# Performance work log

Hardware: AMD Instinct MI355X
Metric: run time of the kernel (lower is better)

The kernel has to match this reference:

```python
import jax, jax.numpy as jnp
import numpy as np

EMBED_DIM = 1024
NUM_HEADS = 16
HEAD_DIM = EMBED_DIM // NUM_HEADS


def setup_inputs() -> dict:
    key = jax.random.key(0)
    ks = jax.random.split(key, 9)
    B, S, E, H, D = 4, 1024, EMBED_DIM, NUM_HEADS, HEAD_DIM
    s = 1.0 / np.sqrt(E)
    return {
        "input_ids": jax.random.normal(ks[0], (B, S, E), dtype=jnp.float32),
        # stacked per-head projection weights, [H, E, D] (x @ W convention)
        "W_q": jax.random.normal(ks[1], (H, E, D), dtype=jnp.float32) * s,
        "b_q": jax.random.normal(ks[2], (H, D), dtype=jnp.float32) * 0.02,
        "W_k": jax.random.normal(ks[3], (H, E, D), dtype=jnp.float32) * s,
        "b_k": jax.random.normal(ks[4], (H, D), dtype=jnp.float32) * 0.02,
        # v_net exists in the module but is UNUSED (bug: v = q_net(x)); kept for faithfulness
        "W_v": jax.random.normal(ks[5], (H, E, D), dtype=jnp.float32) * s,
        "b_v": jax.random.normal(ks[6], (H, D), dtype=jnp.float32) * 0.02,
        "W_o": jax.random.normal(ks[7], (E, E), dtype=jnp.float32) * s,
        "b_o": jax.random.normal(ks[8], (E,), dtype=jnp.float32) * 0.02,
    }


def reference(input_ids, W_q, b_q, W_k, b_k, W_v, b_v, W_o, b_o):
    B, S, E = input_ids.shape
    # per-head projections, batched across heads: [B, H, S, D]
    q = jnp.einsum("bse,hed->bhsd", input_ids, W_q) + b_q[None, :, None, :]
    k = jnp.einsum("bse,hed->bhsd", input_ids, W_k) + b_k[None, :, None, :]
    v = q  # faithful to original bug: v = self.q_net(input_ids)
    # faithful to original: scale by sqrt(seq_len) (q.shape[1] of [B,S,D]), not sqrt(head_dim)
    scores = jnp.einsum("bhqd,bhkd->bhqk", q, k) / jnp.sqrt(jnp.asarray(S, input_ids.dtype))
    # faithful to original: softmax over dim=1 of [B, Sq, Sk] -> the query axis (axis=2 here)
    attn = jax.nn.softmax(scores, axis=2)
    out = jnp.einsum("bhqk,bhkd->bhqd", attn, v)  # [B, H, S, D]
    out = out.transpose(0, 2, 1, 3).reshape(B, S, E)  # concat heads
    return out @ W_o + b_o
```

## Files before the change

### kernel.cpp

```cpp
#include <hip/hip_runtime.h>
#include <cstddef>

typedef __attribute__((ext_vector_type(8))) short bf16x8;
typedef __attribute__((ext_vector_type(4))) float f32x4;
typedef __attribute__((ext_vector_type(8))) unsigned short us8;

#define MFMA(a, b, c) __builtin_amdgcn_mfma_f32_16x16x32_bf16((a), (b), (c), 0, 0, 0)

#define KEXC 0.0450842200277256f

__device__ __forceinline__ unsigned short f2bf(float f) {
  union { float f; unsigned int u; } v; v.f = f;
  return (unsigned short)((v.u + 0x7FFFu + ((v.u >> 16) & 1u)) >> 16);
}
__device__ __forceinline__ float bf2f(unsigned short u) {
  union { unsigned int u; float f; } v; v.u = ((unsigned int)u) << 16; return v.f;
}
__device__ __forceinline__ unsigned int pack_bf2(float a, float b) {
  union { float f; unsigned int u; } x, y; x.f = a; y.f = b;
  return ((x.u + 0x8000u) >> 16) | ((y.u + 0x8000u) & 0xFFFF0000u);
}
__device__ __forceinline__ void glds16(const void* g, void* l) {
  __builtin_amdgcn_global_load_lds(
      (const __attribute__((address_space(1))) unsigned int*)g,
      (__attribute__((address_space(3))) unsigned int*)l, 16, 0, 0);
}

__global__ __launch_bounds__(256) void prep(
    const float* __restrict__ X,  const float* __restrict__ Wq,
    const float* __restrict__ Wk, const float* __restrict__ Wo,
    unsigned short* __restrict__ Xbf, unsigned short* __restrict__ Wqkt,
    unsigned short* __restrict__ Wot)
{
  __shared__ __align__(16) unsigned short T[64 * 72];
  const int t = threadIdx.x;
  int blk = blockIdx.x;
  if (blk < 4096) {
    int i = (blk * 256 + t) * 4;
    float4 v = *(const float4*)&X[i];
    ushort4 o;
    o.x = f2bf(v.x); o.y = f2bf(v.y); o.z = f2bf(v.z); o.w = f2bf(v.w);
    *(ushort4*)&Xbf[i] = o;
    return;
  }
  blk -= 4096;
  const float* W; unsigned short* dst; int mode; float scale = 1.0f;
  if (blk < 256)      { W = Wq; dst = Wqkt;                 mode = 1; }
  else if (blk < 512) { W = Wk; dst = Wqkt + 1024 * 1024;   mode = 1; scale = KEXC; blk -= 256; }
  else                { W = Wo; dst = Wot;                  mode = 0; blk -= 512; }
  const int K = 1024, N = 1024;
  const int n0 = (blk & 15) * 64, k0 = (blk >> 4) * 64;
  const int kr = t >> 4, n4 = (t & 15) * 4;
  #pragma unroll
  for (int i = 0; i < 4; ++i) {
    const int k = k0 + kr + i * 16;
    const float* src = (mode == 0) ? &W[(size_t)k * N + n0 + n4]
                                   : &W[((size_t)(n0 >> 6) * K + k) * 64 + n4];
    float4 v = *(const float4*)src;
    T[(n4 + 0) * 72 + kr + i * 16] = f2bf(v.x * scale);
    T[(n4 + 1) * 72 + kr + i * 16] = f2bf(v.y * scale);
    T[(n4 + 2) * 72 + kr + i * 16] = f2bf(v.z * scale);
    T[(n4 + 3) * 72 + kr + i * 16] = f2bf(v.w * scale);
  }
  __syncthreads();
  const int n = t >> 2, kc = (t & 3) * 16;
  us8 o0 = *(const us8*)&T[n * 72 + kc];
  us8 o1 = *(const us8*)&T[n * 72 + kc + 8];
  *(us8*)&dst[(size_t)(n0 + n) * K + k0 + kc] = o0;
  *(us8*)&dst[(size_t)(n0 + n) * K + k0 + kc + 8] = o1;
}

template<int SPLIT>
__global__ __launch_bounds__(256) void gemm_m97(
    const unsigned short* __restrict__ A, const unsigned short* __restrict__ Bt,
    const float* __restrict__ bias0, const float* __restrict__ bias1,
    void* __restrict__ out0, void* __restrict__ out1, int N, int K, float bs1)
{
  __shared__ __align__(16) unsigned short Asl[128 * 32];
  __shared__ __align__(16) unsigned short Bsl[128 * 32];
  const int tid = threadIdx.x;
  const int m0 = blockIdx.y * 128, n0 = blockIdx.x * 128;
  const int wave = tid >> 6, lane = tid & 63;
  const int wm = (wave & 1) * 64, wn = (wave >> 1) * 64;
  const int l15 = lane & 15, l4 = lane >> 4;
  const int srow = tid >> 2, scol = (tid & 3) * 8;
  const unsigned short* ga = &A[(size_t)(m0 + srow) * K + scol];
  const unsigned short* gb = &Bt[(size_t)(n0 + srow) * K + scol];
  const size_t half = (size_t)64 * K;

  f32x4 acc[4][4] = {};
  for (int kt = 0; kt < K; kt += 32) {
    __syncthreads();
    glds16(ga + kt,        &Asl[tid * 8]);
    glds16(ga + half + kt, &Asl[(tid + 256) * 8]);
    glds16(gb + kt,        &Bsl[tid * 8]);
    glds16(gb + half + kt, &Bsl[(tid + 256) * 8]);
    __syncthreads();
    bf16x8 af[4], bfv[4];
    #pragma unroll
    for (int mi = 0; mi < 4; ++mi)
      af[mi] = *(const bf16x8*)&Asl[(wm + mi * 16 + l15) * 32 + l4 * 8];
    #pragma unroll
    for (int nj = 0; nj < 4; ++nj)
      bfv[nj] = *(const bf16x8*)&Bsl[(wn + nj * 16 + l15) * 32 + l4 * 8];
    #pragma unroll
    for (int mi = 0; mi < 4; ++mi)
      #pragma unroll
      for (int nj = 0; nj < 4; ++nj)
        acc[mi][nj] = MFMA(af[mi], bfv[nj], acc[mi][nj]);
  }

  #pragma unroll
  for (int mi = 0; mi < 4; ++mi) {
    #pragma unroll
    for (int nj = 0; nj < 4; ++nj) {
      const int row = m0 + wm + mi * 16 + l4 * 4;
      const int col = n0 + wn + nj * 16 + l15;
      if (SPLIT) {
        const int qside = (col < 1024);
        const int lc = qside ? col : col - 1024;
        const float bv = qside ? bias0[lc] : bias1[lc] * bs1;
        unsigned short* dst = qside ? (unsigned short*)out0 : (unsigned short*)out1;
        #pragma unroll
        for (int r = 0; r < 4; ++r)
          dst[(size_t)(row + r) * 1024 + lc] = f2bf(acc[mi][nj][r] + bv);
      } else {
        const float bv = bias0[col];
        #pragma unroll
        for (int r = 0; r < 4; ++r)
          ((float*)out0)[(size_t)(row + r) * N + col] = acc[mi][nj][r] + bv;
      }
    }
  }
}

__global__ __launch_bounds__(256) void cs_vt(
    const unsigned short* __restrict__ Qb, const unsigned short* __restrict__ Kb,
    unsigned short* __restrict__ Vt)
{
  const int S = 1024, E = 1024;
  __shared__ __align__(16) unsigned short Ks[2][64 * 32];
  __shared__ __align__(16) unsigned short Qs[2][2][128 * 32];
  __shared__ __align__(16) unsigned short T[64 * 72];
  __shared__ float Ls[64];
  const int bh = blockIdx.x, b = bh >> 4, h = bh & 15;
  const int k0 = blockIdx.y * 64;
  const int tid = threadIdx.x, wave = tid >> 6, lane = tid & 63;
  const int l15 = lane & 15, l4 = lane >> 4;
  const size_t rowBase = (size_t)b * S;
  const int srow = tid >> 2, scol = (tid & 3) * 8;

  glds16(&Kb[(rowBase + k0 + srow) * E + h * 64 + scol],      &Ks[0][tid * 8]);
  glds16(&Kb[(rowBase + k0 + srow) * E + h * 64 + 32 + scol], &Ks[1][tid * 8]);
  #pragma unroll
  for (int ds = 0; ds < 2; ++ds) {
    glds16(&Qb[(rowBase + srow) * E + h * 64 + ds * 32 + scol],      &Qs[0][ds][tid * 8]);
    glds16(&Qb[(rowBase + 64 + srow) * E + h * 64 + ds * 32 + scol], &Qs[0][ds][(tid + 256) * 8]);
  }

  float Lacc[4] = {};
  for (int it = 0; it < 8; ++it) {
    const int cur = it & 1;
    __syncthreads();
    if (it < 7) {
      const int q1 = (it + 1) * 128;
      #pragma unroll
      for (int ds = 0; ds < 2; ++ds) {
        glds16(&Qb[(rowBase + q1 + srow) * E + h * 64 + ds * 32 + scol],
               &Qs[1 - cur][ds][tid * 8]);
        glds16(&Qb[(rowBase + q1 + 64 + srow) * E + h * 64 + ds * 32 + scol],
               &Qs[1 - cur][ds][(tid + 256) * 8]);
      }
    }
    f32x4 accs[8] = {};
    #pragma unroll
    for (int ds = 0; ds < 2; ++ds) {
      bf16x8 af = *(const bf16x8*)&Ks[ds][(wave * 16 + l15) * 32 + l4 * 8];
      #pragma unroll
      for (int nj = 0; nj < 8; ++nj) {
        bf16x8 bv = *(const bf16x8*)&Qs[cur][ds][(nj * 16 + l15) * 32 + l4 * 8];
        accs[nj] = MFMA(af, bv, accs[nj]);
      }
    }
    #pragma unroll
    for (int nj = 0; nj < 8; ++nj)
      #pragma unroll
      for (int rr = 0; rr < 4; ++rr)
        Lacc[rr] += __builtin_amdgcn_exp2f(accs[nj][rr]);
  }
  #pragma unroll
  for (int off = 1; off < 16; off <<= 1)
    #pragma unroll
    for (int rr = 0; rr < 4; ++rr)
      Lacc[rr] += __shfl_xor(Lacc[rr], off);
  if (l15 == 0) {
    #pragma unroll
    for (int rr = 0; rr < 4; ++rr)
      Ls[wave * 16 + l4 * 4 + rr] = Lacc[rr];
  }
  __syncthreads();

  const int row = tid >> 2, d16 = (tid & 3) * 16;
  const float rl = 1.0f / Ls[row];
  const unsigned short* src = &Qb[(rowBase + k0 + row) * E + h * 64 + d16];
  us8 v0 = *(const us8*)src, v1 = *(const us8*)(src + 8);
  #pragma unroll
  for (int j = 0; j < 8; ++j) T[(d16 + j) * 72 + row]     = f2bf(bf2f(v0[j]) * rl);
  #pragma unroll
  for (int j = 0; j < 8; ++j) T[(d16 + 8 + j) * 72 + row] = f2bf(bf2f(v1[j]) * rl);
  __syncthreads();
  const int d = tid >> 2, kh = (tid & 3) * 16;
  unsigned short* dst = &Vt[((size_t)bh * 64 + d) * S + k0 + kh];
  *(us8*)dst       = *(const us8*)&T[d * 72 + kh];
  *(us8*)(dst + 8) = *(const us8*)&T[d * 72 + kh + 8];
}

__global__ __launch_bounds__(256) void attn_out(
    const unsigned short* __restrict__ Qb, const unsigned short* __restrict__ Kb,
    const unsigned short* __restrict__ VtH, unsigned short* __restrict__ O)
{
  const int S = 1024, E = 1024;
  __shared__ __align__(16) unsigned short Qs[2][128 * 32];
  __shared__ __align__(16) unsigned short Ks[2][2][64 * 32];
  __shared__ __align__(16) unsigned short Vs[2][2][64 * 32];
  __shared__ __align__(16) unsigned short Ps[2][128 * 32];
  const int bh = blockIdx.x, b = bh >> 4, h = bh & 15;
  const int q0 = blockIdx.y * 128;
  const int tid = threadIdx.x, wave = tid >> 6, lane = tid & 63;
  const int l15 = lane & 15, l4 = lane >> 4;
  const size_t rowBase = (size_t)b * S;
  const int srow = tid >> 2, scol = (tid & 3) * 8;
  const unsigned short* gK = &Kb[(rowBase + srow) * E + h * 64 + scol];
  const unsigned short* gV = &VtH[((size_t)bh * 64 + srow) * S + scol];

  #pragma unroll
  for (int ds = 0; ds < 2; ++ds) {
    glds16(&Qb[(rowBase + q0 + srow) * E + h * 64 + ds * 32 + scol],      &Qs[ds][tid * 8]);
    glds16(&Qb[(rowBase + q0 + 64 + srow) * E + h * 64 + ds * 32 + scol], &Qs[ds][(tid + 256) * 8]);
  }
  glds16(gK,      &Ks[0][0][tid * 8]);
  glds16(gK + 32, &Ks[0][1][tid * 8]);
  glds16(gV,      &Vs[0][0][tid * 8]);
  glds16(gV + 32, &Vs[0][1][tid * 8]);

  f32x4 acco[2][4] = {};
  for (int it = 0; it < 16; ++it) {
    const int cur = it & 1, k0 = it * 64;
    __syncthreads();
    if (it < 15) {
      const size_t ko = (size_t)(k0 + 64);
      glds16(gK + ko * E,      &Ks[1 - cur][0][tid * 8]);
      glds16(gK + ko * E + 32, &Ks[1 - cur][1][tid * 8]);
      glds16(gV + ko,          &Vs[1 - cur][0][tid * 8]);
      glds16(gV + ko + 32,     &Vs[1 - cur][1][tid * 8]);
    }
    f32x4 accs[4][2] = {};
    #pragma unroll
    for (int ds = 0; ds < 2; ++ds) {
      bf16x8 bq0 = *(const bf16x8*)&Qs[ds][(wave * 32 + l15) * 32 + l4 * 8];
      bf16x8 bq1 = *(const bf16x8*)&Qs[ds][(wave * 32 + 16 + l15) * 32 + l4 * 8];
      #pragma unroll
      for (int mi = 0; mi < 4; ++mi) {
        bf16x8 ak = *(const bf16x8*)&Ks[cur][ds][(mi * 16 + l15) * 32 + l4 * 8];
        accs[mi][0] = MFMA(ak, bq0, accs[mi][0]);
        accs[mi][1] = MFMA(ak, bq1, accs[mi][1]);
      }
    }
    #pragma unroll
    for (int mi = 0; mi < 4; ++mi) {
      #pragma unroll
      for (int nj = 0; nj < 2; ++nj) {
        const int q = wave * 32 + nj * 16 + l15;
        uint2 pk;
        pk.x = pack_bf2(__builtin_amdgcn_exp2f(accs[mi][nj][0]),
                        __builtin_amdgcn_exp2f(accs[mi][nj][1]));
        pk.y = pack_bf2(__builtin_amdgcn_exp2f(accs[mi][nj][2]),
                        __builtin_amdgcn_exp2f(accs[mi][nj][3]));
        *(uint2*)&Ps[mi >> 1][q * 32 + (mi & 1) * 16 + l4 * 4] = pk;
      }
    }
    #pragma unroll
    for (int ks = 0; ks < 2; ++ks) {
      bf16x8 ap0 = *(const bf16x8*)&Ps[ks][(wave * 32 + l15) * 32 + l4 * 8];
      bf16x8 ap1 = *(const bf16x8*)&Ps[ks][(wave * 32 + 16 + l15) * 32 + l4 * 8];
      #pragma unroll
      for (int nj = 0; nj < 4; ++nj) {
        bf16x8 bv = *(const bf16x8*)&Vs[cur][ks][(nj * 16 + l15) * 32 + l4 * 8];
        acco[0][nj] = MFMA(ap0, bv, acco[0][nj]);
        acco[1][nj] = MFMA(ap1, bv, acco[1][nj]);
      }
    }
  }

  #pragma unroll
  for (int mi2 = 0; mi2 < 2; ++mi2)
    #pragma unroll
    for (int nj = 0; nj < 4; ++nj)
      #pragma unroll
      for (int rr = 0; rr < 4; ++rr)
        O[(rowBase + q0 + wave * 32 + mi2 * 16 + l4 * 4 + rr) * E + h * 64 + nj * 16 + l15] =
            f2bf(acco[mi2][nj][rr]);
}

extern "C" void kernel_launch(void* const* d_in, const int* in_sizes, int n_in,
                              void* d_out, int out_size, void* d_ws, size_t ws_size,
                              hipStream_t stream)
{
  const float* X  = (const float*)d_in[0];
  const float* Wq = (const float*)d_in[1];
  const float* bq = (const float*)d_in[2];
  const float* Wk = (const float*)d_in[3];
  const float* bk = (const float*)d_in[4];
  const float* Wo = (const float*)d_in[7];
  const float* bo = (const float*)d_in[8];

  const int Mr = 4096, E = 1024;
  unsigned short* Xbf  = (unsigned short*)d_ws;
  unsigned short* Wqkt = Xbf  + (size_t)Mr * E;
  unsigned short* Wot  = Wqkt + (size_t)2 * E * E;
  unsigned short* Qb   = Wot  + (size_t)E * E;
  unsigned short* Kb   = Qb   + (size_t)Mr * E;
  unsigned short* Ob   = Kb   + (size_t)Mr * E;
  unsigned short* Vt   = Ob   + (size_t)Mr * E;

  prep<<<dim3(4864), dim3(256), 0, stream>>>(X, Wq, Wk, Wo, Xbf, Wqkt, Wot);

  gemm_m97<1><<<dim3(16, 32), dim3(256), 0, stream>>>(
      Xbf, Wqkt, bq, bk, (void*)Qb, (void*)Kb, 2048, E, KEXC);

  cs_vt<<<dim3(64, 16), dim3(256), 0, stream>>>(Qb, Kb, Vt);
  attn_out<<<dim3(64, 8), dim3(256), 0, stream>>>(Qb, Kb, Vt, Ob);

  gemm_m97<0><<<dim3(8, 32), dim3(256), 0, stream>>>(
      Ob, Wot, bo, nullptr, d_out, nullptr, E, E, 1.0f);
}
```

Baseline: 208.7 us.

## Load Q/K/V MFMA fragments directly from global memory instead of LDS staging

Both attention kernels stop staging Q, K and V tiles through double-buffered shared memory with global_load_lds. Each wave now loads its MFMA operand fragments straight from global memory into registers, and only the P tile still goes through LDS. This removes the per-iteration __syncthreads and the LDS traffic, and frees LDS so more blocks can fit. In exchange, every wave redundantly loads the shared K/V tiles, there is no prefetch overlap, and register pressure rises.

```diff
diff --git a/kernel.cpp b/kernel.cpp
--- a/kernel.cpp
+++ b/kernel.cpp
@@ -139,8 +139,6 @@
     unsigned short* __restrict__ Vt)
 {
   const int S = 1024, E = 1024;
-  __shared__ __align__(16) unsigned short Ks[2][64 * 32];
-  __shared__ __align__(16) unsigned short Qs[2][2][128 * 32];
   __shared__ __align__(16) unsigned short T[64 * 72];
   __shared__ float Ls[64];
   const int bh = blockIdx.x, b = bh >> 4, h = bh & 15;
@@ -148,40 +146,28 @@
   const int tid = threadIdx.x, wave = tid >> 6, lane = tid & 63;
   const int l15 = lane & 15, l4 = lane >> 4;
   const size_t rowBase = (size_t)b * S;
-  const int srow = tid >> 2, scol = (tid & 3) * 8;
-
-  glds16(&Kb[(rowBase + k0 + srow) * E + h * 64 + scol],      &Ks[0][tid * 8]);
-  glds16(&Kb[(rowBase + k0 + srow) * E + h * 64 + 32 + scol], &Ks[1][tid * 8]);
-  #pragma unroll
-  for (int ds = 0; ds < 2; ++ds) {
-    glds16(&Qb[(rowBase + srow) * E + h * 64 + ds * 32 + scol],      &Qs[0][ds][tid * 8]);
-    glds16(&Qb[(rowBase + 64 + srow) * E + h * 64 + ds * 32 + scol], &Qs[0][ds][(tid + 256) * 8]);
-  }
+  const unsigned short* gQ = &Qb[rowBase * E + h * 64 + l4 * 8];
+  const unsigned short* gK = &Kb[rowBase * E + h * 64 + l4 * 8];
+
+  bf16x8 ak[2];
+  #pragma unroll
+  for (int ds = 0; ds < 2; ++ds)
+    ak[ds] = *(const bf16x8*)&gK[(size_t)(k0 + wave * 16 + l15) * E + ds * 32];
 
   float Lacc[4] = {};
-  for (int it = 0; it < 8; ++it) {
-    const int cur = it & 1;
-    __syncthreads();
-    if (it < 7) {
-      const int q1 = (it + 1) * 128;
-      #pragma unroll
-      for (int ds = 0; ds < 2; ++ds) {
-        glds16(&Qb[(rowBase + q1 + srow) * E + h * 64 + ds * 32 + scol],
-               &Qs[1 - cur][ds][tid * 8]);
-        glds16(&Qb[(rowBase + q1 + 64 + srow) * E + h * 64 + ds * 32 + scol],
-               &Qs[1 - cur][ds][(tid + 256) * 8]);
-      }
-    }
+  for (int qc = 0; qc < 8; ++qc) {
+    bf16x8 bq[8][2];
+    #pragma unroll
+    for (int nj = 0; nj < 8; ++nj)
+      #pragma unroll
+      for (int ds = 0; ds < 2; ++ds)
+        bq[nj][ds] = *(const bf16x8*)&gQ[(size_t)(qc * 128 + nj * 16 + l15) * E + ds * 32];
     f32x4 accs[8] = {};
     #pragma unroll
-    for (int ds = 0; ds < 2; ++ds) {
-      bf16x8 af = *(const bf16x8*)&Ks[ds][(wave * 16 + l15) * 32 + l4 * 8];
-      #pragma unroll
-      for (int nj = 0; nj < 8; ++nj) {
-        bf16x8 bv = *(const bf16x8*)&Qs[cur][ds][(nj * 16 + l15) * 32 + l4 * 8];
-        accs[nj] = MFMA(af, bv, accs[nj]);
-      }
-    }
+    for (int ds = 0; ds < 2; ++ds)
+      #pragma unroll
+      for (int nj = 0; nj < 8; ++nj)
+        accs[nj] = MFMA(ak[ds], bq[nj][ds], accs[nj]);
     #pragma unroll
     for (int nj = 0; nj < 8; ++nj)
       #pragma unroll
@@ -220,86 +206,80 @@
     const unsigned short* __restrict__ VtH, unsigned short* __restrict__ O)
 {
   const int S = 1024, E = 1024;
-  __shared__ __align__(16) unsigned short Qs[2][128 * 32];
-  __shared__ __align__(16) unsigned short Ks[2][2][64 * 32];
-  __shared__ __align__(16) unsigned short Vs[2][2][64 * 32];
   __shared__ __align__(16) unsigned short Ps[2][128 * 32];
   const int bh = blockIdx.x, b = bh >> 4, h = bh & 15;
   const int q0 = blockIdx.y * 128;
   const int tid = threadIdx.x, wave = tid >> 6, lane = tid & 63;
   const int l15 = lane & 15, l4 = lane >> 4;
   const size_t rowBase = (size_t)b * S;
-  const int srow = tid >> 2, scol = (tid & 3) * 8;
-  const unsigned short* gK = &Kb[(rowBase + srow) * E + h * 64 + scol];
-  const unsigned short* gV = &VtH[((size_t)bh * 64 + srow) * S + scol];
-
-  #pragma unroll
-  for (int ds = 0; ds < 2; ++ds) {
-    glds16(&Qb[(rowBase + q0 + srow) * E + h * 64 + ds * 32 + scol],      &Qs[ds][tid * 8]);
-    glds16(&Qb[(rowBase + q0 + 64 + srow) * E + h * 64 + ds * 32 + scol], &Qs[ds][(tid + 256) * 8]);
-  }
-  glds16(gK,      &Ks[0][0][tid * 8]);
-  glds16(gK + 32, &Ks[0][1][tid * 8]);
-  glds16(gV,      &Vs[0][0][tid * 8]);
-  glds16(gV + 32, &Vs[0][1][tid * 8]);
+  const unsigned short* gQ = &Qb[(rowBase + q0) * E + h * 64 + l4 * 8];
+  const unsigned short* gK = &Kb[rowBase * E + h * 64 + l4 * 8];
+  const unsigned short* gV = &VtH[(size_t)bh * 64 * S + l4 * 8];
+
+  bf16x8 bq[2][2];
+  #pragma unroll
+  for (int nj2 = 0; nj2 < 2; ++nj2)
+    #pragma unroll
+    for (int ds = 0; ds < 2; ++ds)
+      bq[nj2][ds] = *(const bf16x8*)&gQ[(size_t)(wave * 32 + nj2 * 16 + l15) * E + ds * 32];
 
   f32x4 acco[2][4] = {};
   for (int it = 0; it < 16; ++it) {
-    const int cur = it & 1, k0 = it * 64;
-    __syncthreads();
-    if (it < 15) {
-      const size_t ko = (size_t)(k0 + 64);
-      glds16(gK + ko * E,      &Ks[1 - cur][0][tid * 8]);
-      glds16(gK + ko * E + 32, &Ks[1 - cur][1][tid * 8]);
-      glds16(gV + ko,          &Vs[1 - cur][0][tid * 8]);
-      glds16(gV + ko + 32,     &Vs[1 - cur][1][tid * 8]);
-    }
+    const int k0 = it * 64;
+    bf16x8 ak[4][2], bv[4][2];
+    #pragma unroll
+    for (int mi = 0; mi < 4; ++mi)
+      #pragma unroll
+      for (int ds = 0; ds < 2; ++ds)
+        ak[mi][ds] = *(const bf16x8*)&gK[(size_t)(k0 + mi * 16 + l15) * E + ds * 32];
+    #pragma unroll
+    for (int nj = 0; nj < 4; ++nj)
+      #pragma unroll
+      for (int ks = 0; ks < 2; ++ks)
+        bv[nj][ks] = *(const bf16x8*)&gV[(size_t)(nj * 16 + l15) * S + k0 + ks * 32];
+
     f32x4 accs[4][2] = {};
     #pragma unroll
-    for (int ds = 0; ds < 2; ++ds) {
-      bf16x8 bq0 = *(const bf16x8*)&Qs[ds][(wave * 32 + l15) * 32 + l4 * 8];
-      bf16x8 bq1 = *(const bf16x8*)&Qs[ds][(wave * 32 + 16 + l15) * 32 + l4 * 8];
-      #pragma unroll
-      for (int mi = 0; mi < 4; ++mi) {
-        bf16x8 ak = *(const bf16x8*)&Ks[cur][ds][(mi * 16 + l15) * 32 + l4 * 8];
-        accs[mi][0] = MFMA(ak, bq0, accs[mi][0]);
-        accs[mi][1] = MFMA(ak, bq1, accs[mi][1]);
-      }
-    }
+    for (int ds = 0; ds < 2; ++ds)
+      #pragma unroll
+      for (int mi = 0; mi < 4; ++mi)
+        #pragma unroll
+        for (int nj2 = 0; nj2 < 2; ++nj2)
+          accs[mi][nj2] = MFMA(ak[mi][ds], bq[nj2][ds], accs[mi][nj2]);
+
     #pragma unroll
     for (int mi = 0; mi < 4; ++mi) {
       #pragma unroll
-      for (int nj = 0; nj < 2; ++nj) {
-        const int q = wave * 32 + nj * 16 + l15;
+      for (int nj2 = 0; nj2 < 2; ++nj2) {
+        const int q = wave * 32 + nj2 * 16 + l15;
         uint2 pk;
-        pk.x = pack_bf2(__builtin_amdgcn_exp2f(accs[mi][nj][0]),
-                        __builtin_amdgcn_exp2f(accs[mi][nj][1]));
-        pk.y = pack_bf2(__builtin_amdgcn_exp2f(accs[mi][nj][2]),
-                        __builtin_amdgcn_exp2f(accs[mi][nj][3]));
+        pk.x = pack_bf2(__builtin_amdgcn_exp2f(accs[mi][nj2][0]),
+                        __builtin_amdgcn_exp2f(accs[mi][nj2][1]));
+        pk.y = pack_bf2(__builtin_amdgcn_exp2f(accs[mi][nj2][2]),
+                        __builtin_amdgcn_exp2f(accs[mi][nj2][3]));
         *(uint2*)&Ps[mi >> 1][q * 32 + (mi & 1) * 16 + l4 * 4] = pk;
       }
     }
     #pragma unroll
     for (int ks = 0; ks < 2; ++ks) {
-      bf16x8 ap0 = *(const bf16x8*)&Ps[ks][(wave * 32 + l15) * 32 + l4 * 8];
-      bf16x8 ap1 = *(const bf16x8*)&Ps[ks][(wave * 32 + 16 + l15) * 32 + l4 * 8];
-      #pragma unroll
-      for (int nj = 0; nj < 4; ++nj) {
-        bf16x8 bv = *(const bf16x8*)&Vs[cur][ks][(nj * 16 + l15) * 32 + l4 * 8];
-        acco[0][nj] = MFMA(ap0, bv, acco[0][nj]);
-        acco[1][nj] = MFMA(ap1, bv, acco[1][nj]);
+      #pragma unroll
+      for (int nj2 = 0; nj2 < 2; ++nj2) {
+        bf16x8 ap = *(const bf16x8*)&Ps[ks][(wave * 32 + nj2 * 16 + l15) * 32 + l4 * 8];
+        #pragma unroll
+        for (int nj = 0; nj < 4; ++nj)
+          acco[nj2][nj] = MFMA(ap, bv[nj][ks], acco[nj2][nj]);
       }
     }
   }
 
   #pragma unroll
-  for (int mi2 = 0; mi2 < 2; ++mi2)
+  for (int nj2 = 0; nj2 < 2; ++nj2)
     #pragma unroll
     for (int nj = 0; nj < 4; ++nj)
       #pragma unroll
       for (int rr = 0; rr < 4; ++rr)
-        O[(rowBase + q0 + wave * 32 + mi2 * 16 + l4 * 4 + rr) * E + h * 64 + nj * 16 + l15] =
-            f2bf(acco[mi2][nj][rr]);
+        O[(rowBase + q0 + wave * 32 + nj2 * 16 + l4 * 4 + rr) * E + h * 64 + nj * 16 + l15] =
+            f2bf(acco[nj2][nj][rr]);
 }
 
 extern "C" void kernel_launch(void* const* d_in, const int* in_sizes, int n_in,
```

After: 269.3 us. 1.29x slower.
